# Performance work log

Measured on AMD Instinct MI355X. Metric: run time of the kernel, lower is better.

## Reference

```python
import jax, jax.numpy as jnp
import numpy as np

D_MODEL = 1024
H = 16
D_K = D_MODEL // H
B, S = 2, 2048
NEG = -1.0e9


def setup_inputs() -> dict:
    key = jax.random.key(0)
    ks = jax.random.split(key, 9)
    sc = 1.0 / np.sqrt(D_MODEL)
    x = jax.random.normal(ks[0], (B, S, D_MODEL), dtype=jnp.float32)
    mask = jnp.tril(jnp.ones((S, S), dtype=jnp.int32))[None, None]  # causal [1,1,S,S]
    Wq = jax.random.normal(ks[1], (D_MODEL, D_MODEL), jnp.float32) * sc
    bq = jnp.zeros((D_MODEL,), jnp.float32)
    Wk = jax.random.normal(ks[2], (D_MODEL, D_MODEL), jnp.float32) * sc
    bk = jnp.zeros((D_MODEL,), jnp.float32)
    Wv = jax.random.normal(ks[3], (D_MODEL, D_MODEL), jnp.float32) * sc
    bv = jnp.zeros((D_MODEL,), jnp.float32)
    Wo = jax.random.normal(ks[4], (D_MODEL, D_MODEL), jnp.float32) * sc
    bo = jnp.zeros((D_MODEL,), jnp.float32)
    return {"x": x, "mask": mask, "Wq": Wq, "bq": bq, "Wk": Wk, "bk": bk,
            "Wv": Wv, "bv": bv, "Wo": Wo, "bo": bo}


def reference(x, mask, Wq, bq, Wk, bk, Wv, bv, Wo, bo):
    Bx, Sx, _ = x.shape
    # QKV projections (nn.Linear: x @ W.T + b)
    q = (x @ Wq.T + bq).reshape(Bx, Sx, H, D_K).transpose(0, 2, 1, 3)  # [B,h,S,dk]
    k = (x @ Wk.T + bk).reshape(Bx, Sx, H, D_K).transpose(0, 2, 1, 3)
    v = (x @ Wv.T + bv).reshape(Bx, Sx, H, D_K).transpose(0, 2, 1, 3)
    scores = jnp.einsum('bhqd,bhkd->bhqk', q, k) / np.sqrt(D_K)  # [B,h,S,S]
    scores = jnp.where(mask == 0, NEG, scores)
    attn = jax.nn.softmax(scores, axis=-1)  # dropout p=0 -> identity
    out = jnp.einsum('bhqk,bhkd->bhqd', attn, v)
    out = out.transpose(0, 2, 1, 3).reshape(Bx, Sx, H * D_K)
    return out @ Wo.T + bo
```

## Files before the change

kernel.cpp:

```cpp
#include <hip/hip_runtime.h>
#include <hip/hip_bf16.h>

typedef __bf16 bf16;
typedef bf16 bf16x8 __attribute__((ext_vector_type(8)));
typedef bf16 bf16x4 __attribute__((ext_vector_type(4)));
typedef float f32x4 __attribute__((ext_vector_type(4)));
typedef unsigned int u32;

#define S_LEN 2048
#define DM 1024
#define NH 16
#define DK 64
#define MTOK 4096

__device__ __forceinline__ void gld16(const void* g, void* l) {
  __builtin_amdgcn_global_load_lds(
      (const __attribute__((address_space(1))) u32*)g,
      (__attribute__((address_space(3))) u32*)l, 16, 0, 0);
}

__global__ __launch_bounds__(256) void cvt_all(
    const float* __restrict__ x, const float* __restrict__ wq, const float* __restrict__ wk,
    const float* __restrict__ wv, const float* __restrict__ wo,
    bf16* __restrict__ xb, bf16* __restrict__ wqb, bf16* __restrict__ wkb,
    bf16* __restrict__ wvb, bf16* __restrict__ wob) {
  const int i = blockIdx.x * blockDim.x + threadIdx.x;
  const int NX = (MTOK * DM) / 4;
  const int NW = (DM * DM) / 4;
  const float* src;
  bf16* dst;
  int off;
  if (i < NX) {
    src = x; dst = xb; off = i;
  } else {
    const int j = i - NX;
    const int w = j >> 18;
    off = j & (NW - 1);
    src = (w == 0) ? wq : (w == 1) ? wk : (w == 2) ? wv : wo;
    dst = (w == 0) ? wqb : (w == 1) ? wkb : (w == 2) ? wvb : wob;
  }
  f32x4 v = reinterpret_cast<const f32x4*>(src)[off];
  bf16x4 o;
  o[0] = (bf16)v[0]; o[1] = (bf16)v[1]; o[2] = (bf16)v[2]; o[3] = (bf16)v[3];
  reinterpret_cast<bf16x4*>(dst)[off] = o;
}

__global__ __launch_bounds__(256) void gemm_qkv(
    const bf16* __restrict__ A,
    const bf16* __restrict__ Wq, const bf16* __restrict__ Wk, const bf16* __restrict__ Wv,
    const float* __restrict__ Bq, const float* __restrict__ Bk, const float* __restrict__ Bv,
    bf16* __restrict__ Qo, bf16* __restrict__ Ko, bf16* __restrict__ Vt) {
  __shared__ char smem[65536];
  const int z = blockIdx.z;
  const bf16* W = (z == 0) ? Wq : (z == 1) ? Wk : Wv;
  const float* bias = (z == 0) ? Bq : (z == 1) ? Bk : Bv;
  const int m0 = blockIdx.y * 128;
  const int n0 = blockIdx.x * 128;
  const int tid = threadIdx.x;
  const int lane = tid & 63;
  const int wid = tid >> 6;
  const int wr = (wid >> 1) * 64, wc = (wid & 1) * 64;
  const int scb = 16 * ((lane & 7) ^ (lane >> 3));
  const int lr8 = lane >> 3;

  f32x4 acc[4][4] = {};

  auto STAGE = [&](int bi, int k0) {
#pragma unroll
    for (int c = 0; c < 4; ++c) {
      const int chunk = wid * 4 + c;
      const int row = chunk * 8 + lr8;
      gld16((const char*)A + ((size_t)(m0 + row) * DM + k0) * 2 + scb,
            smem + bi * 32768 + chunk * 1024);
      gld16((const char*)W + ((size_t)(n0 + row) * DM + k0) * 2 + scb,
            smem + bi * 32768 + 16384 + chunk * 1024);
    }
  };

  STAGE(0, 0);
  asm volatile("s_waitcnt vmcnt(0)" ::: "memory");
  __builtin_amdgcn_s_barrier();

  const int NK = DM / 64;
  for (int it = 0; it < NK; ++it) {
    if (it + 1 < NK) STAGE((it + 1) & 1, (it + 1) * 64);
    const char* As = smem + (it & 1) * 32768;
    const char* Bs = As + 16384;
#pragma unroll
    for (int kk = 0; kk < 2; ++kk) {
      bf16x8 af[4], bfr[4];
#pragma unroll
      for (int i = 0; i < 4; ++i) {
        const int ar = wr + i * 16 + (lane & 15);
        af[i] = *reinterpret_cast<const bf16x8*>(
            As + ar * 128 + ((kk * 64 + 16 * (lane >> 4)) ^ ((ar & 7) << 4)));
        const int br = wc + i * 16 + (lane & 15);
        bfr[i] = *reinterpret_cast<const bf16x8*>(
            Bs + br * 128 + ((kk * 64 + 16 * (lane >> 4)) ^ ((br & 7) << 4)));
      }
      __builtin_amdgcn_s_setprio(1);
#pragma unroll
      for (int i = 0; i < 4; ++i)
#pragma unroll
        for (int j = 0; j < 4; ++j)
          acc[i][j] = __builtin_amdgcn_mfma_f32_16x16x32_bf16(af[i], bfr[j], acc[i][j], 0, 0, 0);
      __builtin_amdgcn_s_setprio(0);
    }
    asm volatile("s_waitcnt vmcnt(0)" ::: "memory");
    __builtin_amdgcn_s_barrier();
  }

  const float QSC = 0.125f * 1.44269504089f;
  const int bIdx = m0 >> 11;
  const int r4 = (lane >> 4) * 4;
#pragma unroll
  for (int i = 0; i < 4; ++i) {
    const int mrow = m0 + wr + i * 16 + r4;
    const int srow = mrow & (S_LEN - 1);
#pragma unroll
    for (int j = 0; j < 4; ++j) {
      const int n = n0 + wc + j * 16 + (lane & 15);
      const int h = n >> 6, d = n & 63;
      const int bh = bIdx * NH + h;
      const float bs = bias[n];
      if (z == 0) {
#pragma unroll
        for (int r = 0; r < 4; ++r)
          Qo[((size_t)bh * S_LEN + srow + r) * DK + d] = (bf16)((acc[i][j][r] + bs) * QSC);
      } else if (z == 1) {
#pragma unroll
        for (int r = 0; r < 4; ++r)
          Ko[((size_t)bh * S_LEN + srow + r) * DK + d] = (bf16)(acc[i][j][r] + bs);
      } else {
        bf16x4 pk;
#pragma unroll
        for (int r = 0; r < 4; ++r) pk[r] = (bf16)(acc[i][j][r] + bs);
        *reinterpret_cast<bf16x4*>(&Vt[((size_t)bh * DK + d) * S_LEN + srow]) = pk;
      }
    }
  }
}

__global__ __launch_bounds__(512) void attn_fwd(
    const bf16* __restrict__ Q, const bf16* __restrict__ K,
    const bf16* __restrict__ Vt, bf16* __restrict__ O) {
  __shared__ char smem[65536];

  const int bid = blockIdx.x;
  const int qt = (S_LEN / 128 - 1) - (bid >> 5);
  const int bh = bid & 31;
  const int tid = threadIdx.x, lane = tid & 63, wid = tid >> 6;
  const int q0 = qt * 128;
  const int scb = 16 * ((lane & 7) ^ (lane >> 3));
  const int l15 = lane & 15;
  const int lg = lane >> 4;
  const int r4 = lg * 4;

  const bf16* qbase = Q + ((size_t)bh * S_LEN + q0 + wid * 16) * DK;
  bf16x8 qf[2];
#pragma unroll
  for (int kk = 0; kk < 2; ++kk)
    qf[kk] = *reinterpret_cast<const bf16x8*>(qbase + l15 * DK + kk * 32 + 8 * lg);

  f32x4 o[4] = {};
  float m_r[4], l_r[4];
#pragma unroll
  for (int r = 0; r < 4; ++r) { m_r[r] = -3.0e38f; l_r[r] = 0.f; }

  const int nt = 2 * (qt + 1);

  auto STAGE = [&](int bi, int t) {
    const int kv0 = t * 64;
    const int row = wid * 8 + (lane >> 3);
    gld16((const char*)K + ((size_t)(bh * S_LEN + kv0 + row)) * 128 + scb,
          smem + bi * 16384 + wid * 1024);
    gld16((const char*)Vt + ((size_t)(bh * DK + row)) * (S_LEN * 2) + (size_t)kv0 * 2 + scb,
          smem + bi * 16384 + 8192 + wid * 1024);
  };

  STAGE(0, 0);
  char* pw = smem + 49152 + wid * 2048;

  for (int t = 0; t < nt; ++t) {
    const int kv0 = t * 64;
    if (t + 1 < nt) {
      STAGE((t + 1) % 3, t + 1);
      asm volatile("s_waitcnt vmcnt(2)" ::: "memory");
    } else {
      asm volatile("s_waitcnt vmcnt(0)" ::: "memory");
    }
    __builtin_amdgcn_s_barrier();
    asm volatile("" ::: "memory");
    const char* Kc = smem + (t % 3) * 16384;
    const char* Vc = Kc + 8192;

    f32x4 sf[4] = {};
#pragma unroll
    for (int kk = 0; kk < 2; ++kk) {
      bf16x8 bb[4];
#pragma unroll
      for (int j = 0; j < 4; ++j) {
        const int kr = j * 16 + l15;
        bb[j] = *reinterpret_cast<const bf16x8*>(
            Kc + kr * 128 + ((kk * 64 + 16 * lg) ^ ((kr & 7) << 4)));
      }
      __builtin_amdgcn_s_setprio(1);
#pragma unroll
      for (int j = 0; j < 4; ++j)
        sf[j] = __builtin_amdgcn_mfma_f32_16x16x32_bf16(qf[kk], bb[j], sf[j], 0, 0, 0);
      __builtin_amdgcn_s_setprio(0);
    }

    if (t >= nt - 2) {
#pragma unroll
      for (int j = 0; j < 4; ++j) {
        const int key = kv0 + j * 16 + l15;
#pragma unroll
        for (int r = 0; r < 4; ++r) {
          const int qrow = q0 + wid * 16 + r4 + r;
          if (key > qrow) sf[j][r] = -1.0e9f;
        }
      }
    }

#pragma unroll
    for (int r = 0; r < 4; ++r) {
      float mx = fmaxf(fmaxf(sf[0][r], sf[1][r]), fmaxf(sf[2][r], sf[3][r]));
      mx = fmaxf(mx, __shfl_xor(mx, 1));
      mx = fmaxf(mx, __shfl_xor(mx, 2));
      mx = fmaxf(mx, __shfl_xor(mx, 4));
      mx = fmaxf(mx, __shfl_xor(mx, 8));
      if (mx > m_r[r] + 8.f) {
        const float sc = exp2f(m_r[r] - mx);
        l_r[r] *= sc;
#pragma unroll
        for (int j = 0; j < 4; ++j) o[j][r] *= sc;
        m_r[r] = mx;
      }
      const float m_new = m_r[r];
      float rs = 0.f;
#pragma unroll
      for (int j = 0; j < 4; ++j) {
        const float p = exp2f(sf[j][r] - m_new);
        sf[j][r] = p;
        rs += p;
      }
      rs += __shfl_xor(rs, 1);
      rs += __shfl_xor(rs, 2);
      rs += __shfl_xor(rs, 4);
      rs += __shfl_xor(rs, 8);
      l_r[r] += rs;
    }

#pragma unroll
    for (int r = 0; r < 4; ++r) {
      const int pr = r4 + r;
      const int sw = (pr & 7) << 4;
#pragma unroll
      for (int j = 0; j < 4; ++j)
        *reinterpret_cast<bf16*>(pw + pr * 128 + ((j * 32 + 2 * l15) ^ sw)) = (bf16)sf[j][r];
    }

#pragma unroll
    for (int kk = 0; kk < 2; ++kk) {
      bf16x8 vb[4];
#pragma unroll
      for (int j = 0; j < 4; ++j) {
        const int vr = j * 16 + l15;
        vb[j] = *reinterpret_cast<const bf16x8*>(
            Vc + vr * 128 + ((kk * 64 + 16 * lg) ^ ((vr & 7) << 4)));
      }
      const bf16x8 pa = *reinterpret_cast<const bf16x8*>(
          pw + l15 * 128 + ((kk * 64 + 16 * lg) ^ ((l15 & 7) << 4)));
      __builtin_amdgcn_s_setprio(1);
#pragma unroll
      for (int j = 0; j < 4; ++j)
        o[j] = __builtin_amdgcn_mfma_f32_16x16x32_bf16(pa, vb[j], o[j], 0, 0, 0);
      __builtin_amdgcn_s_setprio(0);
    }
  }

  const int b = bh >> 4, h = bh & 15;
#pragma unroll
  for (int r = 0; r < 4; ++r) {
    const float inv = 1.0f / l_r[r];
    const int srow = q0 + wid * 16 + r4 + r;
    bf16* obase = O + ((size_t)(b * S_LEN + srow)) * DM + h * DK;
#pragma unroll
    for (int j = 0; j < 4; ++j) obase[j * 16 + l15] = (bf16)(o[j][r] * inv);
  }
}

__global__ __launch_bounds__(256) void gemm_out(
    const bf16* __restrict__ A, const bf16* __restrict__ W,
    const float* __restrict__ bias, float* __restrict__ C) {
  __shared__ char smem[65536];
  const int m0 = blockIdx.y * 128, n0 = blockIdx.x * 128;
  const int tid = threadIdx.x, lane = tid & 63, wid = tid >> 6;
  const int wr = (wid >> 1) * 64, wc = (wid & 1) * 64;
  const int scb = 16 * ((lane & 7) ^ (lane >> 3));
  const int lr8 = lane >> 3;
  f32x4 acc[4][4] = {};

  auto STAGE = [&](int bi, int k0) {
#pragma unroll
    for (int c = 0; c < 4; ++c) {
      const int chunk = wid * 4 + c;
      const int row = chunk * 8 + lr8;
      gld16((const char*)A + ((size_t)(m0 + row) * DM + k0) * 2 + scb,
            smem + bi * 32768 + chunk * 1024);
      gld16((const char*)W + ((size_t)(n0 + row) * DM + k0) * 2 + scb,
            smem + bi * 32768 + 16384 + chunk * 1024);
    }
  };

  STAGE(0, 0);
  asm volatile("s_waitcnt vmcnt(0)" ::: "memory");
  __builtin_amdgcn_s_barrier();

  const int NK = DM / 64;
  for (int it = 0; it < NK; ++it) {
    if (it + 1 < NK) STAGE((it + 1) & 1, (it + 1) * 64);
    const char* As = smem + (it & 1) * 32768;
    const char* Bs = As + 16384;
#pragma unroll
    for (int kk = 0; kk < 2; ++kk) {
      bf16x8 af[4], bfr[4];
#pragma unroll
      for (int i = 0; i < 4; ++i) {
        const int ar = wr + i * 16 + (lane & 15);
        af[i] = *reinterpret_cast<const bf16x8*>(
            As + ar * 128 + ((kk * 64 + 16 * (lane >> 4)) ^ ((ar & 7) << 4)));
        const int br = wc + i * 16 + (lane & 15);
        bfr[i] = *reinterpret_cast<const bf16x8*>(
            Bs + br * 128 + ((kk * 64 + 16 * (lane >> 4)) ^ ((br & 7) << 4)));
      }
      __builtin_amdgcn_s_setprio(1);
#pragma unroll
      for (int i = 0; i < 4; ++i)
#pragma unroll
        for (int j = 0; j < 4; ++j)
          acc[i][j] = __builtin_amdgcn_mfma_f32_16x16x32_bf16(af[i], bfr[j], acc[i][j], 0, 0, 0);
      __builtin_amdgcn_s_setprio(0);
    }
    asm volatile("s_waitcnt vmcnt(0)" ::: "memory");
    __builtin_amdgcn_s_barrier();
  }

  const int r4 = (lane >> 4) * 4;
#pragma unroll
  for (int i = 0; i < 4; ++i) {
    const int mrow = m0 + wr + i * 16 + r4;
#pragma unroll
    for (int j = 0; j < 4; ++j) {
      const int n = n0 + wc + j * 16 + (lane & 15);
      const float bs = bias[n];
#pragma unroll
      for (int r = 0; r < 4; ++r) C[(size_t)(mrow + r) * DM + n] = acc[i][j][r] + bs;
    }
  }
}

extern "C" void kernel_launch(void* const* d_in, const int* in_sizes, int n_in,
                              void* d_out, int out_size, void* d_ws, size_t ws_size,
                              hipStream_t stream) {
  const float* x = (const float*)d_in[0];
  const float* Wq = (const float*)d_in[2];
  const float* bq = (const float*)d_in[3];
  const float* Wk = (const float*)d_in[4];
  const float* bk = (const float*)d_in[5];
  const float* Wv = (const float*)d_in[6];
  const float* bv = (const float*)d_in[7];
  const float* Wo = (const float*)d_in[8];
  const float* bo = (const float*)d_in[9];

  char* ws = (char*)d_ws;
  bf16* xb  = (bf16*)(ws);
  bf16* wqb = (bf16*)(ws + (8u << 20));
  bf16* wkb = (bf16*)(ws + (10u << 20));
  bf16* wvb = (bf16*)(ws + (12u << 20));
  bf16* wob = (bf16*)(ws + (14u << 20));
  bf16* Qw  = (bf16*)(ws + (16u << 20));
  bf16* Kw  = (bf16*)(ws + (24u << 20));
  bf16* Vtw = (bf16*)(ws + (32u << 20));
  bf16* AO  = (bf16*)(ws + (40u << 20));

  cvt_all<<<8192, 256, 0, stream>>>(x, Wq, Wk, Wv, Wo, xb, wqb, wkb, wvb, wob);

  gemm_qkv<<<dim3(DM / 128, MTOK / 128, 3), 256, 0, stream>>>(
      xb, wqb, wkb, wvb, bq, bk, bv, Qw, Kw, Vtw);
  attn_fwd<<<dim3((S_LEN / 128) * 32), 512, 0, stream>>>(Qw, Kw, Vtw, AO);
  gemm_out<<<dim3(DM / 128, MTOK / 128), 256, 0, stream>>>(AO, wob, bo, (float*)d_out);
}
```

Measured before the change: 136.7 us.

## Rewrite attention with 32x32 MFMA transposed scores and register-resident P

The attention kernel now computes S^T with 32x32x16 bf16 MFMAs, so each lane owns one query row. The row max and sum need a single cross-half shuffle instead of four-step butterfly reductions. P is packed to bf16 in registers and rearranged with v_permlane32_swap instead of a round trip through LDS. Blocks drop to 4 waves of 32 rows each, LDS shrinks to 48KB, and the output is written as bf16x4 vectors. The risks are higher register pressure from the 16-wide accumulators and fewer waves per block to hide latency.

Measured after the change: 118.6 us. 13.2% less time.

```diff
diff --git a/kernel.cpp b/kernel.cpp
--- a/kernel.cpp
+++ b/kernel.cpp
@@ -5,7 +5,9 @@
 typedef bf16 bf16x8 __attribute__((ext_vector_type(8)));
 typedef bf16 bf16x4 __attribute__((ext_vector_type(4)));
 typedef float f32x4 __attribute__((ext_vector_type(4)));
+typedef float f32x16 __attribute__((ext_vector_type(16)));
 typedef unsigned int u32;
+typedef u32 u32x4 __attribute__((ext_vector_type(4)));
 
 #define S_LEN 2048
 #define DM 1024
@@ -17,6 +19,15 @@
   __builtin_amdgcn_global_load_lds(
       (const __attribute__((address_space(1))) u32*)g,
       (__attribute__((address_space(3))) u32*)l, 16, 0, 0);
+}
+
+__device__ __forceinline__ u32 pkbf(float lo, float hi) {
+  union { bf16 h[2]; u32 u; } c;
+  c.h[0] = (bf16)lo; c.h[1] = (bf16)hi;
+  return c.u;
+}
+__device__ __forceinline__ void plswap(u32& a, u32& b) {
+  asm volatile("v_permlane32_swap_b32 %0, %1" : "+v"(a), "+v"(b));
 }
 
 __global__ __launch_bounds__(256) void cvt_all(
@@ -141,51 +152,53 @@
   }
 }
 
-__global__ __launch_bounds__(512) void attn_fwd(
+__global__ __launch_bounds__(256) void attn_fwd(
     const bf16* __restrict__ Q, const bf16* __restrict__ K,
     const bf16* __restrict__ Vt, bf16* __restrict__ O) {
-  __shared__ char smem[65536];
+  __shared__ char smem[49152];
 
   const int bid = blockIdx.x;
-  const int qt = (S_LEN / 128 - 1) - (bid >> 5);
+  const int qt = 15 - (bid >> 5);
   const int bh = bid & 31;
   const int tid = threadIdx.x, lane = tid & 63, wid = tid >> 6;
   const int q0 = qt * 128;
   const int scb = 16 * ((lane & 7) ^ (lane >> 3));
-  const int l15 = lane & 15;
-  const int lg = lane >> 4;
-  const int r4 = lg * 4;
-
-  const bf16* qbase = Q + ((size_t)bh * S_LEN + q0 + wid * 16) * DK;
-  bf16x8 qf[2];
-#pragma unroll
-  for (int kk = 0; kk < 2; ++kk)
-    qf[kk] = *reinterpret_cast<const bf16x8*>(qbase + l15 * DK + kk * 32 + 8 * lg);
-
-  f32x4 o[4] = {};
-  float m_r[4], l_r[4];
-#pragma unroll
-  for (int r = 0; r < 4; ++r) { m_r[r] = -3.0e38f; l_r[r] = 0.f; }
+  const int l31 = lane & 31;
+  const int hi = lane >> 5;
+  const int qrow = q0 + wid * 32 + l31;
+  const int swz = (l31 & 7) << 4;
+
+  const bf16* qb = Q + ((size_t)bh * S_LEN + qrow) * DK;
+  bf16x8 qf[4];
+#pragma unroll
+  for (int ks = 0; ks < 4; ++ks)
+    qf[ks] = *reinterpret_cast<const bf16x8*>(qb + ks * 16 + 8 * hi);
+
+  f32x16 o0 = {}, o1 = {};
+  float m_r = -3.0e38f, l_r = 0.f;
 
   const int nt = 2 * (qt + 1);
 
   auto STAGE = [&](int bi, int t) {
     const int kv0 = t * 64;
-    const int row = wid * 8 + (lane >> 3);
-    gld16((const char*)K + ((size_t)(bh * S_LEN + kv0 + row)) * 128 + scb,
-          smem + bi * 16384 + wid * 1024);
-    gld16((const char*)Vt + ((size_t)(bh * DK + row)) * (S_LEN * 2) + (size_t)kv0 * 2 + scb,
-          smem + bi * 16384 + 8192 + wid * 1024);
+#pragma unroll
+    for (int c = 0; c < 2; ++c) {
+      const int chunk = wid * 2 + c;
+      const int row = chunk * 8 + (lane >> 3);
+      gld16((const char*)K + ((size_t)(bh * S_LEN + kv0 + row)) * 128 + scb,
+            smem + bi * 16384 + chunk * 1024);
+      gld16((const char*)Vt + ((size_t)(bh * DK + row)) * (S_LEN * 2) + (size_t)kv0 * 2 + scb,
+            smem + bi * 16384 + 8192 + chunk * 1024);
+    }
   };
 
   STAGE(0, 0);
-  char* pw = smem + 49152 + wid * 2048;
 
   for (int t = 0; t < nt; ++t) {
     const int kv0 = t * 64;
     if (t + 1 < nt) {
       STAGE((t + 1) % 3, t + 1);
-      asm volatile("s_waitcnt vmcnt(2)" ::: "memory");
+      asm volatile("s_waitcnt vmcnt(4)" ::: "memory");
     } else {
       asm volatile("s_waitcnt vmcnt(0)" ::: "memory");
     }
@@ -194,100 +207,100 @@
     const char* Kc = smem + (t % 3) * 16384;
     const char* Vc = Kc + 8192;
 
-    f32x4 sf[4] = {};
-#pragma unroll
-    for (int kk = 0; kk < 2; ++kk) {
-      bf16x8 bb[4];
-#pragma unroll
-      for (int j = 0; j < 4; ++j) {
-        const int kr = j * 16 + l15;
-        bb[j] = *reinterpret_cast<const bf16x8*>(
-            Kc + kr * 128 + ((kk * 64 + 16 * lg) ^ ((kr & 7) << 4)));
+    f32x16 s0 = {}, s1 = {};
+#pragma unroll
+    for (int kt = 0; kt < 2; ++kt) {
+      bf16x8 ka[4];
+#pragma unroll
+      for (int ks = 0; ks < 4; ++ks)
+        ka[ks] = *reinterpret_cast<const bf16x8*>(
+            Kc + (kt * 32 + l31) * 128 + ((ks * 32 + 16 * hi) ^ swz));
+      f32x16& sd = kt ? s1 : s0;
+      __builtin_amdgcn_s_setprio(1);
+#pragma unroll
+      for (int ks = 0; ks < 4; ++ks)
+        sd = __builtin_amdgcn_mfma_f32_32x32x16_bf16(ka[ks], qf[ks], sd, 0, 0, 0);
+      __builtin_amdgcn_s_setprio(0);
+    }
+
+    if (t >= nt - 2) {
+#pragma unroll
+      for (int r = 0; r < 16; ++r) {
+        const int key0 = kv0 + (r & 3) + 8 * (r >> 2) + 4 * hi;
+        if (key0 > qrow) s0[r] = -1.0e9f;
+        if (key0 + 32 > qrow) s1[r] = -1.0e9f;
       }
+    }
+
+    float mx = s0[0];
+#pragma unroll
+    for (int r = 1; r < 16; ++r) mx = fmaxf(mx, s0[r]);
+#pragma unroll
+    for (int r = 0; r < 16; ++r) mx = fmaxf(mx, s1[r]);
+    mx = fmaxf(mx, __shfl_xor(mx, 32));
+    if (!__all(mx <= m_r + 8.f)) {
+      const float nm = fmaxf(m_r, mx);
+      const float sc = exp2f(m_r - nm);
+      l_r *= sc;
+      o0 *= sc;
+      o1 *= sc;
+      m_r = nm;
+    }
+    float rs = 0.f;
+#pragma unroll
+    for (int r = 0; r < 16; ++r) { s0[r] = exp2f(s0[r] - m_r); rs += s0[r]; }
+#pragma unroll
+    for (int r = 0; r < 16; ++r) { s1[r] = exp2f(s1[r] - m_r); rs += s1[r]; }
+    rs += __shfl_xor(rs, 32);
+    l_r += rs;
+
+    bf16x8 pb[4];
+#pragma unroll
+    for (int kt = 0; kt < 2; ++kt) {
+      const f32x16& p = kt ? s1 : s0;
+#pragma unroll
+      for (int s2 = 0; s2 < 2; ++s2) {
+        u32 cA = pkbf(p[8 * s2 + 0], p[8 * s2 + 1]);
+        u32 cB = pkbf(p[8 * s2 + 2], p[8 * s2 + 3]);
+        u32 cC = pkbf(p[8 * s2 + 4], p[8 * s2 + 5]);
+        u32 cD = pkbf(p[8 * s2 + 6], p[8 * s2 + 7]);
+        plswap(cA, cC);
+        plswap(cB, cD);
+        u32x4 w;
+        w[0] = cA; w[1] = cB; w[2] = cC; w[3] = cD;
+        pb[kt * 2 + s2] = __builtin_bit_cast(bf16x8, w);
+      }
+    }
+
+#pragma unroll
+    for (int dt = 0; dt < 2; ++dt) {
+      bf16x8 va[4];
+#pragma unroll
+      for (int ks = 0; ks < 4; ++ks)
+        va[ks] = *reinterpret_cast<const bf16x8*>(
+            Vc + (dt * 32 + l31) * 128 + ((ks * 32 + 16 * hi) ^ swz));
+      f32x16& od = dt ? o1 : o0;
       __builtin_amdgcn_s_setprio(1);
 #pragma unroll
-      for (int j = 0; j < 4; ++j)
-        sf[j] = __builtin_amdgcn_mfma_f32_16x16x32_bf16(qf[kk], bb[j], sf[j], 0, 0, 0);
+      for (int ks = 0; ks < 4; ++ks)
+        od = __builtin_amdgcn_mfma_f32_32x32x16_bf16(va[ks], pb[ks], od, 0, 0, 0);
       __builtin_amdgcn_s_setprio(0);
     }
-
-    if (t >= nt - 2) {
-#pragma unroll
-      for (int j = 0; j < 4; ++j) {
-        const int key = kv0 + j * 16 + l15;
-#pragma unroll
-        for (int r = 0; r < 4; ++r) {
-          const int qrow = q0 + wid * 16 + r4 + r;
-          if (key > qrow) sf[j][r] = -1.0e9f;
-        }
-      }
-    }
-
-#pragma unroll
-    for (int r = 0; r < 4; ++r) {
-      float mx = fmaxf(fmaxf(sf[0][r], sf[1][r]), fmaxf(sf[2][r], sf[3][r]));
-      mx = fmaxf(mx, __shfl_xor(mx, 1));
-      mx = fmaxf(mx, __shfl_xor(mx, 2));
-      mx = fmaxf(mx, __shfl_xor(mx, 4));
-      mx = fmaxf(mx, __shfl_xor(mx, 8));
-      if (mx > m_r[r] + 8.f) {
-        const float sc = exp2f(m_r[r] - mx);
-        l_r[r] *= sc;
-#pragma unroll
-        for (int j = 0; j < 4; ++j) o[j][r] *= sc;
-        m_r[r] = mx;
-      }
-      const float m_new = m_r[r];
-      float rs = 0.f;
-#pragma unroll
-      for (int j = 0; j < 4; ++j) {
-        const float p = exp2f(sf[j][r] - m_new);
-        sf[j][r] = p;
-        rs += p;
-      }
-      rs += __shfl_xor(rs, 1);
-      rs += __shfl_xor(rs, 2);
-      rs += __shfl_xor(rs, 4);
-      rs += __shfl_xor(rs, 8);
-      l_r[r] += rs;
-    }
-
-#pragma unroll
-    for (int r = 0; r < 4; ++r) {
-      const int pr = r4 + r;
-      const int sw = (pr & 7) << 4;
-#pragma unroll
-      for (int j = 0; j < 4; ++j)
-        *reinterpret_cast<bf16*>(pw + pr * 128 + ((j * 32 + 2 * l15) ^ sw)) = (bf16)sf[j][r];
-    }
-
-#pragma unroll
-    for (int kk = 0; kk < 2; ++kk) {
-      bf16x8 vb[4];
-#pragma unroll
-      for (int j = 0; j < 4; ++j) {
-        const int vr = j * 16 + l15;
-        vb[j] = *reinterpret_cast<const bf16x8*>(
-            Vc + vr * 128 + ((kk * 64 + 16 * lg) ^ ((vr & 7) << 4)));
-      }
-      const bf16x8 pa = *reinterpret_cast<const bf16x8*>(
-          pw + l15 * 128 + ((kk * 64 + 16 * lg) ^ ((l15 & 7) << 4)));
-      __builtin_amdgcn_s_setprio(1);
-#pragma unroll
-      for (int j = 0; j < 4; ++j)
-        o[j] = __builtin_amdgcn_mfma_f32_16x16x32_bf16(pa, vb[j], o[j], 0, 0, 0);
-      __builtin_amdgcn_s_setprio(0);
-    }
   }
 
   const int b = bh >> 4, h = bh & 15;
-#pragma unroll
-  for (int r = 0; r < 4; ++r) {
-    const float inv = 1.0f / l_r[r];
-    const int srow = q0 + wid * 16 + r4 + r;
-    bf16* obase = O + ((size_t)(b * S_LEN + srow)) * DM + h * DK;
-#pragma unroll
-    for (int j = 0; j < 4; ++j) obase[j * 16 + l15] = (bf16)(o[j][r] * inv);
+  const float inv = 1.0f / l_r;
+  bf16* obase = O + ((size_t)(b * S_LEN + qrow)) * DM + h * DK;
+#pragma unroll
+  for (int dt = 0; dt < 2; ++dt) {
+    const f32x16& od = dt ? o1 : o0;
+#pragma unroll
+    for (int g = 0; g < 4; ++g) {
+      bf16x4 pk4;
+#pragma unroll
+      for (int m = 0; m < 4; ++m) pk4[m] = (bf16)(od[4 * g + m] * inv);
+      *reinterpret_cast<bf16x4*>(obase + dt * 32 + 8 * g + 4 * hi) = pk4;
+    }
   }
 }
 
@@ -389,6 +402,6 @@
 
   gemm_qkv<<<dim3(DM / 128, MTOK / 128, 3), 256, 0, stream>>>(
       xb, wqb, wkb, wvb, bq, bk, bv, Qw, Kw, Vtw);
-  attn_fwd<<<dim3((S_LEN / 128) * 32), 512, 0, stream>>>(Qw, Kw, Vtw, AO);
+  attn_fwd<<<dim3(512), 256, 0, stream>>>(Qw, Kw, Vtw, AO);
   gemm_out<<<dim3(DM / 128, MTOK / 128), 256, 0, stream>>>(AO, wob, bo, (float*)d_out);
 }
```
